# Kernel optimization log

Hardware: AMD Instinct MI355X
Metric: run time of the kernel (lower is better)

## Reference

```python
import jax, jax.numpy as jnp
import numpy as np

B, S, D, H = 2, 2048, 1024, 16
HD = D // H  # head_dim = 64


def setup_inputs() -> dict:
    key = jax.random.key(0)
    ks = jax.random.split(key, 6)
    scale = 0.02
    x = jax.random.normal(ks[0], (B, S, D), dtype=jnp.float32)
    Wq = jax.random.normal(ks[1], (D, D), dtype=jnp.float32) * scale
    Wk = jax.random.normal(ks[2], (D, D), dtype=jnp.float32) * scale
    Wv = jax.random.normal(ks[3], (D, D), dtype=jnp.float32) * scale
    Wo = jax.random.normal(ks[4], (D, D), dtype=jnp.float32) * scale
    bo = jnp.zeros((D,), dtype=jnp.float32)
    return {"x": x, "Wq": Wq, "Wk": Wk, "Wv": Wv, "Wo": Wo, "bo": bo}


def reference(x, Wq, Wk, Wv, Wo, bo):
    b, s, _ = x.shape
    # Linear projections (qkv_bias=False), split into heads: [b, h, s, hd]
    def split_heads(t):
        return t.reshape(b, s, H, HD).transpose(0, 2, 1, 3)
    q = split_heads(x @ Wq)
    k = split_heads(x @ Wk)
    v = split_heads(x @ Wv)
    # Scaled dot-product scores: [b, h, s, s]
    scores = jnp.einsum('bhqd,bhkd->bhqk', q, k) / jnp.sqrt(jnp.float32(HD))
    # Causal mask: triu(ones, diagonal=1) positions -> -inf
    causal = jnp.triu(jnp.ones((s, s), dtype=bool), k=1)
    scores = jnp.where(causal, -jnp.inf, scores)
    attn = jax.nn.softmax(scores, axis=-1)
    # dropout p=0.0 (eval-equivalent): identity
    ctx = jnp.einsum('bhqk,bhkd->bhqd', attn, v)  # [b, h, s, hd]
    ctx = ctx.transpose(0, 2, 1, 3).reshape(b, s, D)
    return ctx @ Wo + bo
```

## Files before the change

kernel.cpp:

```cpp
#include <hip/hip_runtime.h>
#include <math.h>

#define BB 2
#define SS 2048
#define DD 1024
#define HH 16
#define HD 64
#define MM (BB * SS)

typedef __bf16 bf16;
typedef __attribute__((ext_vector_type(8))) __bf16 bf16x8;
typedef __attribute__((ext_vector_type(4))) __bf16 bf16x4;
typedef __attribute__((ext_vector_type(4))) short short4v;
typedef __attribute__((ext_vector_type(4))) float f32x4;

#if __has_builtin(__builtin_amdgcn_exp2f)
#define EXP2F(x) __builtin_amdgcn_exp2f(x)
#else
#define EXP2F(x) exp2f(x)
#endif

__device__ __forceinline__ f32x4 pv_mfma16(bf16x4 a, short4v b, f32x4 c) {
    return __builtin_amdgcn_mfma_f32_16x16x16bf16_1k(
        __builtin_bit_cast(short4v, a), b, c, 0, 0, 0);
}

__device__ __forceinline__ void gld_lds16(const void* g, void* l) {
    __builtin_amdgcn_global_load_lds(
        (const __attribute__((address_space(1))) void*)g,
        (__attribute__((address_space(3))) void*)l, 16, 0, 0);
}

__global__ __launch_bounds__(256) void prep(
    const float* __restrict__ x,
    const float* __restrict__ W0, const float* __restrict__ W1,
    const float* __restrict__ W2, const float* __restrict__ W3,
    bf16* __restrict__ xb, bf16* __restrict__ Wt)
{
    __shared__ float tile[32][33];
    const int z = blockIdx.z;
    if (z < 4) {
        const float* W = (z == 0) ? W0 : (z == 1) ? W1 : (z == 2) ? W2 : W3;
        bf16* O = Wt + (size_t)z * DD * DD;
        const int tx = threadIdx.x & 31, ty = threadIdx.x >> 5;
        const int k0 = blockIdx.y * 32, n0 = blockIdx.x * 32;
#pragma unroll
        for (int i = 0; i < 4; ++i)
            tile[ty + i * 8][tx] = W[(size_t)(k0 + ty + i * 8) * DD + n0 + tx];
        __syncthreads();
#pragma unroll
        for (int i = 0; i < 4; ++i)
            O[(size_t)(n0 + ty + i * 8) * DD + k0 + tx] = (bf16)tile[tx][ty + i * 8];
    } else {
        const int lb = (z - 4) * 1024 + blockIdx.y * 32 + blockIdx.x;
        const size_t i = ((size_t)lb * 256 + threadIdx.x) * 8;
        const float4 a = *(const float4*)(x + i);
        const float4 b = *(const float4*)(x + i + 4);
        bf16x8 o;
        o[0] = (bf16)a.x; o[1] = (bf16)a.y; o[2] = (bf16)a.z; o[3] = (bf16)a.w;
        o[4] = (bf16)b.x; o[5] = (bf16)b.y; o[6] = (bf16)b.z; o[7] = (bf16)b.w;
        *(bf16x8*)(xb + i) = o;
    }
}

template <int SWAP>
__device__ __forceinline__ void mfma_core(
    const bf16* __restrict__ A, const bf16* __restrict__ Bt,
    int bm, int bn, int K, bf16* As, bf16* Bs, f32x4 (&acc)[4][4])
{
    const int t = threadIdx.x;
    const int w = t >> 6;
    const int l16 = t & 15, quad = (t >> 4) & 3;
    const int wr = w >> 1, wc = w & 1;
    const int arow = t >> 2;
    const int achk = (((t & 3) ^ ((t >> 3) & 3)) << 3);

    const bf16* gA = A + (size_t)(bm + arow) * K + achk;
    const bf16* gB = Bt + (size_t)(bn + arow) * K + achk;
    bf16* lA = As + w * 512;
    bf16* lB = Bs + w * 512;

    const int swz = (l16 >> 1) & 3;
    int offA[4], offB[4];
#pragma unroll
    for (int i = 0; i < 4; ++i) {
        offA[i] = (wr * 64 + i * 16 + l16) * 32 + ((quad ^ swz) << 3);
        offB[i] = (wc * 64 + i * 16 + l16) * 32 + ((quad ^ swz) << 3);
    }

#define GSTAGE(BUF, KO) do {                                                  \
        gld_lds16(gA + (KO),                  lA + (BUF) * 4096);             \
        gld_lds16(gA + (size_t)64 * K + (KO), lA + (BUF) * 4096 + 2048);      \
        gld_lds16(gB + (KO),                  lB + (BUF) * 4096);             \
        gld_lds16(gB + (size_t)64 * K + (KO), lB + (BUF) * 4096 + 2048);      \
    } while (0)

#define GCOMPUTE(BUF) do {                                                    \
        const bf16* Ab = As + (BUF) * 4096;                                   \
        const bf16* Bb = Bs + (BUF) * 4096;                                   \
        bf16x8 af[4], bv[4];                                                  \
        _Pragma("unroll")                                                     \
        for (int i = 0; i < 4; ++i) {                                         \
            af[i] = *(const bf16x8*)(Ab + offA[i]);                           \
            bv[i] = *(const bf16x8*)(Bb + offB[i]);                           \
        }                                                                     \
        _Pragma("unroll")                                                     \
        for (int mi = 0; mi < 4; ++mi)                                        \
            _Pragma("unroll")                                                 \
            for (int ni = 0; ni < 4; ++ni)                                    \
                acc[mi][ni] = SWAP                                            \
                    ? __builtin_amdgcn_mfma_f32_16x16x32_bf16(                \
                          bv[ni], af[mi], acc[mi][ni], 0, 0, 0)               \
                    : __builtin_amdgcn_mfma_f32_16x16x32_bf16(                \
                          af[mi], bv[ni], acc[mi][ni], 0, 0, 0);              \
    } while (0)

#define GBAR() do {                                                           \
        asm volatile("s_barrier" ::: "memory");                               \
        __builtin_amdgcn_sched_barrier(0);                                    \
    } while (0)

    GSTAGE(0, 0);
    const int nk = K >> 5;
    for (int kt = 0; kt < nk; kt += 2) {
        GSTAGE(1, (kt + 1) << 5);
        asm volatile("s_waitcnt vmcnt(4)" ::: "memory");
        GBAR();
        GCOMPUTE(0);
        asm volatile("s_waitcnt lgkmcnt(0)" ::: "memory");
        GBAR();
        if (kt + 2 < nk) {
            GSTAGE(0, (kt + 2) << 5);
            asm volatile("s_waitcnt vmcnt(4)" ::: "memory");
        } else {
            asm volatile("s_waitcnt vmcnt(0)" ::: "memory");
        }
        GBAR();
        GCOMPUTE(1);
        asm volatile("s_waitcnt lgkmcnt(0)" ::: "memory");
        GBAR();
    }
#undef GBAR
#undef GCOMPUTE
#undef GSTAGE
}

__global__ __launch_bounds__(256) void gemm_qkv(
    const bf16* __restrict__ xb, const bf16* __restrict__ Wt,
    bf16* __restrict__ Qb, bf16* __restrict__ Kb, bf16* __restrict__ Vb)
{
    __shared__ __align__(16) bf16 As[2 * 128 * 32];
    __shared__ __align__(16) bf16 Bs[2 * 128 * 32];
    const int bm = blockIdx.y * 128, bn = blockIdx.x * 128, z = blockIdx.z;

    const int t = threadIdx.x;
    const int w = t >> 6, l16 = t & 15, quad = (t >> 4) & 3;
    const int wr = w >> 1, wc = w & 1;

    f32x4 acc[4][4] = {};
    if (z < 2) {
        mfma_core<1>(xb, Wt + (size_t)z * DD * DD, bm, bn, DD, As, Bs, acc);
        bf16* outp = (z == 0) ? Qb : Kb;
        const float scl = (z == 0) ? 0.18033688011f : 1.0f;
#pragma unroll
        for (int mi = 0; mi < 4; ++mi) {
            const int srow = bm + wr * 64 + mi * 16 + l16;
            const int b = srow >> 11, s = srow & (SS - 1);
#pragma unroll
            for (int ni = 0; ni < 4; ++ni) {
                const int colb = bn + wc * 64 + ni * 16 + quad * 4;
                const int h = colb >> 6, hd = colb & 63;
                bf16x4 o;
#pragma unroll
                for (int r = 0; r < 4; ++r) o[r] = (bf16)(acc[mi][ni][r] * scl);
                *(bf16x4*)(outp + ((size_t)((b * HH + h) * SS + s)) * HD + hd) = o;
            }
        }
    } else {
        mfma_core<0>(xb, Wt + (size_t)2 * DD * DD, bm, bn, DD, As, Bs, acc);
#pragma unroll
        for (int mi = 0; mi < 4; ++mi) {
            const int srow0 = bm + wr * 64 + mi * 16 + quad * 4;
            const int b = srow0 >> 11, s0 = srow0 & (SS - 1);
#pragma unroll
            for (int ni = 0; ni < 4; ++ni) {
                const int col = bn + wc * 64 + ni * 16 + l16;
                const int h = col >> 6, hd = col & 63;
                bf16x4 o;
#pragma unroll
                for (int r = 0; r < 4; ++r) o[r] = (bf16)acc[mi][ni][r];
                *(bf16x4*)(Vb + ((size_t)((b * HH + h) * HD + hd)) * SS + s0) = o;
            }
        }
    }
}

__global__ __launch_bounds__(256) void gemm_out(
    const bf16* __restrict__ ctx, const bf16* __restrict__ Wto,
    const float* __restrict__ bias, float* __restrict__ out)
{
    __shared__ __align__(16) bf16 As[2 * 128 * 32];
    __shared__ __align__(16) bf16 Bs[2 * 128 * 32];
    const int bm = blockIdx.y * 128, bn = blockIdx.x * 128;

    f32x4 acc[4][4] = {};
    mfma_core<1>(ctx, Wto, bm, bn, DD, As, Bs, acc);

    const int t = threadIdx.x;
    const int w = t >> 6, l16 = t & 15, quad = (t >> 4) & 3;
    const int wr = w >> 1, wc = w & 1;

#pragma unroll
    for (int mi = 0; mi < 4; ++mi) {
        const int row = bm + wr * 64 + mi * 16 + l16;
#pragma unroll
        for (int ni = 0; ni < 4; ++ni) {
            const int colb = bn + wc * 64 + ni * 16 + quad * 4;
            const float4 b4 = *(const float4*)(bias + colb);
            float4 o;
            o.x = acc[mi][ni][0] + b4.x;
            o.y = acc[mi][ni][1] + b4.y;
            o.z = acc[mi][ni][2] + b4.z;
            o.w = acc[mi][ni][3] + b4.w;
            *(float4*)(out + (size_t)row * DD + colb) = o;
        }
    }
}

__global__ __launch_bounds__(512, 4) void attn_flash(
    const bf16* __restrict__ Q, const bf16* __restrict__ K,
    const bf16* __restrict__ Vt, bf16* __restrict__ ctx)
{
    __shared__ __align__(16) bf16 Ks[2][64 * 64];
    __shared__ __align__(16) bf16 Vs[2][64 * 64];

    const int t = threadIdx.x;
    const int w = t >> 6;
    const int lane = t & 63;
    const int l16 = lane & 15, quad = lane >> 4;

    const int L  = blockIdx.x;
    const int bh = L & 31;
    const int slot = L >> 5;
    const int g = (slot < 8) ? 15 - slot : slot - 8;
    const int q0b = g * 128;
    const int q0w = q0b + w * 16;
    const int qrow = q0w + l16;
    const int nkt = 2 * g + 2;

    const bf16* Qp = Q  + ((size_t)bh * SS + q0w) * HD;
    const bf16* Kp = K  + (size_t)bh * SS * HD;
    const bf16* Vp = Vt + (size_t)bh * HD * SS;

    const bf16x8 bQ0 = *(const bf16x8*)(Qp + l16 * HD + quad * 8);
    const bf16x8 bQ1 = *(const bf16x8*)(Qp + l16 * HD + 32 + quad * 8);

    const int srow = w * 8 + (lane >> 3);
    const int c = ((lane & 7) - srow) & 7;
    const bf16* gK = Kp + (size_t)srow * HD + c * 8;
    const bf16* gV = Vp + (size_t)srow * SS + c * 8;
    bf16* const lK = &Ks[0][w * 512];
    bf16* const lV = &Vs[0][w * 512];

#define STAGE(BUF, KB) do {                                              \
        gld_lds16(gK + (size_t)(KB) * HD, lK + (BUF) * 4096);            \
        gld_lds16(gV + (KB),              lV + (BUF) * 4096);            \
    } while (0)

    const int offK0 = l16 * 64 + ((quad + l16) & 7) * 8;
    const int offK1 = l16 * 64 + ((quad + 4 + l16) & 7) * 8;
    int offV[4];
#pragma unroll
    for (int mi = 0; mi < 4; ++mi)
        offV[mi] = l16 * 64 + ((((quad >> 1) + 2 * mi + l16) & 7) * 8)
                 + (quad & 1) * 4;

    const bf16* const KsB = &Ks[0][0];
    const bf16* const VsB = &Vs[0][0];

    f32x4 accO[4] = {{0,0,0,0},{0,0,0,0},{0,0,0,0},{0,0,0,0}};
    float Lr = 0.f;

#define TILE(BUF, KB) do {                                                   \
        f32x4 St[4] = {{0,0,0,0},{0,0,0,0},{0,0,0,0},{0,0,0,0}};             \
        _Pragma("unroll")                                                    \
        for (int mi = 0; mi < 4; ++mi) {                                     \
            const bf16x8 a0 = *(const bf16x8*)(KsB + (BUF) * 4096            \
                                               + mi * 1024 + offK0);         \
            const bf16x8 a1 = *(const bf16x8*)(KsB + (BUF) * 4096            \
                                               + mi * 1024 + offK1);         \
            St[mi] = __builtin_amdgcn_mfma_f32_16x16x32_bf16(                \
                a0, bQ0, St[mi], 0, 0, 0);                                   \
            St[mi] = __builtin_amdgcn_mfma_f32_16x16x32_bf16(                \
                a1, bQ1, St[mi], 0, 0, 0);                                   \
        }                                                                    \
        if ((KB) + 63 > q0w) {                                               \
            _Pragma("unroll")                                                \
            for (int mi = 0; mi < 4; ++mi)                                   \
                _Pragma("unroll")                                            \
                for (int rr = 0; rr < 4; ++rr)                               \
                    if ((KB) + mi * 16 + quad * 4 + rr > qrow)               \
                        St[mi][rr] = -1e30f;                                 \
        }                                                                    \
        float rs = 0.f;                                                      \
        short4v pb[4];                                                       \
        _Pragma("unroll")                                                    \
        for (int mi = 0; mi < 4; ++mi) {                                     \
            bf16x4 pk;                                                       \
            _Pragma("unroll")                                                \
            for (int rr = 0; rr < 4; ++rr) {                                 \
                const float p = EXP2F(St[mi][rr]);                           \
                rs += p;                                                     \
                pk[rr] = (bf16)p;                                            \
            }                                                                \
            pb[mi] = __builtin_bit_cast(short4v, pk);                        \
        }                                                                    \
        rs += __shfl_xor(rs, 16);                                            \
        rs += __shfl_xor(rs, 32);                                            \
        Lr += rs;                                                            \
        _Pragma("unroll")                                                    \
        for (int mi = 0; mi < 4; ++mi) {                                     \
            _Pragma("unroll")                                                 \
            for (int db = 0; db < 4; ++db) {                                 \
                const bf16x4 aV = *(const bf16x4*)(VsB + (BUF) * 4096        \
                                                   + db * 1024 + offV[mi]);  \
                accO[db] = pv_mfma16(aV, pb[mi], accO[db]);                  \
            }                                                                \
        }                                                                    \
    } while (0)

    STAGE(0, 0);
    int kb = 0;
    for (int kt = 0; kt < nkt; kt += 2) {
        __syncthreads();
        STAGE(1, kb + 64);
        TILE(0, kb);
        __syncthreads();
        if (kt + 2 < nkt) {
            STAGE(0, kb + 128);
            TILE(1, kb + 64);
        } else {
            if (w >= 4) TILE(1, kb + 64);
        }
        kb += 128;
    }
#undef TILE
#undef STAGE

    const float rinv = 1.0f / Lr;
    const int b = bh >> 4, h = bh & (HH - 1);
    bf16* op = ctx + ((size_t)(b * SS + q0w + l16)) * DD + h * HD;
#pragma unroll
    for (int db = 0; db < 4; ++db) {
        bf16x4 o;
#pragma unroll
        for (int rr = 0; rr < 4; ++rr) o[rr] = (bf16)(accO[db][rr] * rinv);
        *(bf16x4*)(op + db * 16 + quad * 4) = o;
    }
}

extern "C" void kernel_launch(void* const* d_in, const int* in_sizes, int n_in,
                              void* d_out, int out_size, void* d_ws, size_t ws_size,
                              hipStream_t stream)
{
    const float* x  = (const float*)d_in[0];
    const float* Wq = (const float*)d_in[1];
    const float* Wk = (const float*)d_in[2];
    const float* Wv = (const float*)d_in[3];
    const float* Wo = (const float*)d_in[4];
    const float* bo = (const float*)d_in[5];
    float* out = (float*)d_out;

    const size_t chunk = (size_t)MM * DD;
    bf16* xb  = (bf16*)d_ws;
    bf16* Wt  = xb + chunk;
    bf16* Qb  = Wt + 4 * (size_t)DD * DD;
    bf16* Kb  = Qb + chunk;
    bf16* Vb  = Kb + chunk;
    bf16* ctx = Vb + chunk;

    prep<<<dim3(32, 32, 6), dim3(256), 0, stream>>>(x, Wq, Wk, Wv, Wo, xb, Wt);

    gemm_qkv<<<dim3(DD / 128, MM / 128, 3), dim3(256), 0, stream>>>(xb, Wt, Qb, Kb, Vb);

    attn_flash<<<dim3(BB * HH * (SS / 128)), dim3(512), 0, stream>>>(Qb, Kb, Vb, ctx);

    gemm_out<<<dim3(DD / 128, MM / 128), dim3(256), 0, stream>>>(
        ctx, Wt + 3 * (size_t)DD * DD, bo, out);
}
```

Baseline: 178.0 us.

## Software-pipeline attention PV MFMAs one tile behind QK to overlap softmax

Splits the attention tile into a phase that computes QK scores and exp for the current K/V tile while issuing the previous tile's P·V MFMAs, with V fragments preloaded into registers. This is meant to hide softmax exp latency and LDS V reads behind matrix work. It raises register pressure (16 bf16x4 V fragments plus P held across phases), which may reduce occupancy. A final flush handles the last tile.

```diff
diff --git a/kernel.cpp b/kernel.cpp
--- a/kernel.cpp
+++ b/kernel.cpp
@@ -281,7 +281,10 @@
     f32x4 accO[4] = {{0,0,0,0},{0,0,0,0},{0,0,0,0},{0,0,0,0}};
     float Lr = 0.f;
 
-#define TILE(BUF, KB) do {                                                   \
+    short4v pbr[4];
+    bf16x4  avr[4][4];
+
+#define PHASE(BUF, KB, DOPREV) do {                                          \
         f32x4 St[4] = {{0,0,0,0},{0,0,0,0},{0,0,0,0},{0,0,0,0}};             \
         _Pragma("unroll")                                                    \
         for (int mi = 0; mi < 4; ++mi) {                                     \
@@ -294,6 +297,19 @@
             St[mi] = __builtin_amdgcn_mfma_f32_16x16x32_bf16(                \
                 a1, bQ1, St[mi], 0, 0, 0);                                   \
         }                                                                    \
+        if (DOPREV) {                                                        \
+            _Pragma("unroll")                                                \
+            for (int mi = 0; mi < 4; ++mi)                                   \
+                _Pragma("unroll")                                            \
+                for (int db = 0; db < 4; ++db)                               \
+                    accO[db] = pv_mfma16(avr[mi][db], pbr[mi], accO[db]);    \
+        }                                                                    \
+        _Pragma("unroll")                                                    \
+        for (int mi = 0; mi < 4; ++mi)                                       \
+            _Pragma("unroll")                                                \
+            for (int db = 0; db < 4; ++db)                                   \
+                avr[mi][db] = *(const bf16x4*)(VsB + (BUF) * 4096            \
+                                               + db * 1024 + offV[mi]);      \
         if ((KB) + 63 > q0w) {                                               \
             _Pragma("unroll")                                                \
             for (int mi = 0; mi < 4; ++mi)                                   \
@@ -303,7 +319,6 @@
                         St[mi][rr] = -1e30f;                                 \
         }                                                                    \
         float rs = 0.f;                                                      \
-        short4v pb[4];                                                       \
         _Pragma("unroll")                                                    \
         for (int mi = 0; mi < 4; ++mi) {                                     \
             bf16x4 pk;                                                       \
@@ -313,38 +328,42 @@
                 rs += p;                                                     \
                 pk[rr] = (bf16)p;                                            \
             }                                                                \
-            pb[mi] = __builtin_bit_cast(short4v, pk);                        \
+            pbr[mi] = __builtin_bit_cast(short4v, pk);                       \
         }                                                                    \
         rs += __shfl_xor(rs, 16);                                            \
         rs += __shfl_xor(rs, 32);                                            \
         Lr += rs;                                                            \
+    } while (0)
+
+#define PVFIN() do {                                                         \
         _Pragma("unroll")                                                    \
-        for (int mi = 0; mi < 4; ++mi) {                                     \
-            _Pragma("unroll")                                                 \
-            for (int db = 0; db < 4; ++db) {                                 \
-                const bf16x4 aV = *(const bf16x4*)(VsB + (BUF) * 4096        \
-                                                   + db * 1024 + offV[mi]);  \
-                accO[db] = pv_mfma16(aV, pb[mi], accO[db]);                  \
-            }                                                                \
-        }                                                                    \
+        for (int mi = 0; mi < 4; ++mi)                                       \
+            _Pragma("unroll")                                                \
+            for (int db = 0; db < 4; ++db)                                   \
+                accO[db] = pv_mfma16(avr[mi][db], pbr[mi], accO[db]);        \
     } while (0)
 
     STAGE(0, 0);
-    int kb = 0;
-    for (int kt = 0; kt < nkt; kt += 2) {
+    __syncthreads();
+    STAGE(1, 64);
+    PHASE(0, 0, 0);
+    __syncthreads();
+    if (nkt > 2) STAGE(0, 128);
+    if (nkt > 2 || w >= 4) PHASE(1, 64, 1);
+
+    int kb = 128;
+    for (int kt = 2; kt < nkt; kt += 2) {
         __syncthreads();
         STAGE(1, kb + 64);
-        TILE(0, kb);
+        PHASE(0, kb, 1);
         __syncthreads();
-        if (kt + 2 < nkt) {
-            STAGE(0, kb + 128);
-            TILE(1, kb + 64);
-        } else {
-            if (w >= 4) TILE(1, kb + 64);
-        }
+        if (kt + 2 < nkt) STAGE(0, kb + 128);
+        if (kt + 2 < nkt || w >= 4) PHASE(1, kb + 64, 1);
         kb += 128;
     }
-#undef TILE
+    PVFIN();
+#undef PVFIN
+#undef PHASE
 #undef STAGE
 
     const float rinv = 1.0f / Lr;
```

Measured after the change: 180.0 us. No clear change (+1.2%).
